# Kernel tuning notes

Measured on AMD Instinct MI355X. Metric: run time of the kernel, lower is better.

Reference implementation:

```python
import jax, jax.numpy as jnp
import numpy as np

B, N, D = 2, 256, 128

def _linear(x, W, b):
    # torch nn.Linear: y = x @ W.T + b, W shape (out, in)
    return jnp.einsum('bijd,od->bijo', x, W) + b

def setup_inputs() -> dict:
    key = jax.random.key(0)
    ks = jax.random.split(key, 11)
    s = 0.02
    inp = {
        'ef': jax.random.normal(ks[0], (B, N, N, D), dtype=jnp.float32),
        'Wq': jax.random.normal(ks[1], (D, D), dtype=jnp.float32) * s,
        'bq': jax.random.normal(ks[2], (D,), dtype=jnp.float32) * s,
        'Wk': jax.random.normal(ks[3], (D, D), dtype=jnp.float32) * s,
        'bk': jax.random.normal(ks[4], (D,), dtype=jnp.float32) * s,
        'Wv1': jax.random.normal(ks[5], (D, D), dtype=jnp.float32) * s,
        'bv1': jax.random.normal(ks[6], (D,), dtype=jnp.float32) * s,
        'Wv2': jax.random.normal(ks[7], (D, D), dtype=jnp.float32) * s,
        'bv2': jax.random.normal(ks[8], (D,), dtype=jnp.float32) * s,
        'Wo': jax.random.normal(ks[9], (D, D), dtype=jnp.float32) * s,
        'bo': jax.random.normal(ks[10], (D,), dtype=jnp.float32) * s,
    }
    return inp

def reference(ef, Wq, bq, Wk, bk, Wv1, bv1, Wv2, bv2, Wo, bo):
    d = ef.shape[-1]
    q = _linear(ef, Wq, bq)    # (b,i,l,d)
    k = _linear(ef, Wk, bk)    # (b,l,j,d)
    v1 = _linear(ef, Wv1, bv1) # (b,i,l,d)
    v2 = _linear(ef, Wv2, bv2) # (b,l,j,d)
    # scores over triples (i,l,j): sum_d q[b,i,l,d]*k[b,l,j,d]
    scale = jnp.asarray(1.0 / (d ** 0.5), dtype=ef.dtype)
    qk = jnp.einsum('bild,bljd->bilj', q, k) * scale
    # original softmax is over dim=-2 of (b,i,l,j,1) -> over j
    a = jax.nn.softmax(qk, axis=-1)  # (b,i,l,j)
    # sum_j a[b,i,l,j] * v1[b,i,l,d] * v2[b,l,j,d]
    ctx = jnp.einsum('bilj,bljd->bild', a, v2) * v1  # (b,i,l,d)
    out = _linear(ctx, Wo, bo)
    return out
```

## Files before the change

### kernel.cpp

```cpp
#include <hip/hip_runtime.h>


typedef __bf16 bf16x8 __attribute__((ext_vector_type(8)));
typedef float  f32x4  __attribute__((ext_vector_type(4)));

#define MFMA(a, b, c) __builtin_amdgcn_mfma_f32_16x16x32_bf16((a), (b), (c), 0, 0, 0)

union U8 { bf16x8 v; unsigned int w[4]; };

__device__ __forceinline__ unsigned short rne_bf16(float f) {
  unsigned int u = __float_as_uint(f);
  u += 0x7fffu + ((u >> 16) & 1u);
  return (unsigned short)(u >> 16);
}

__device__ __forceinline__ unsigned int cvt_pk(float lo, float hi) {
  unsigned int r;
  asm("v_cvt_pk_bf16_f32 %0, %1, %2" : "=v"(r) : "v"(lo), "v"(hi));
  return r;
}

__device__ __forceinline__ bf16x8 cvt_frag(const float* __restrict__ p) {
  f32x4 a = *(const f32x4*)p;
  f32x4 b = *(const f32x4*)(p + 4);
  U8 t;
  t.w[0] = cvt_pk(a[0], a[1]);
  t.w[1] = cvt_pk(a[2], a[3]);
  t.w[2] = cvt_pk(b[0], b[1]);
  t.w[3] = cvt_pk(b[2], b[3]);
  return t.v;
}

__device__ __forceinline__ bf16x8 xpose(unsigned int w01a, unsigned int w01b,
                                        unsigned int w23a, unsigned int w23b,
                                        int sa, int sb, bool hi) {
  U8 u;
  { int x0 = __shfl((int)w01a, sa), x1 = __shfl((int)w01b, sa);
    u.w[0] = (unsigned int)(hi ? x1 : x0); }
  { int x0 = __shfl((int)w23a, sa), x1 = __shfl((int)w23b, sa);
    u.w[1] = (unsigned int)(hi ? x1 : x0); }
  { int x0 = __shfl((int)w01a, sb), x1 = __shfl((int)w01b, sb);
    u.w[2] = (unsigned int)(hi ? x1 : x0); }
  { int x0 = __shfl((int)w23a, sb), x1 = __shfl((int)w23b, sb);
    u.w[3] = (unsigned int)(hi ? x1 : x0); }
  return u.v;
}

__device__ __forceinline__ void softmax_pack(f32x4 ST[16], unsigned int p01[16],
                                             unsigned int p23[16]) {
  float t16[16];
  #pragma unroll
  for (int jt = 0; jt < 16; ++jt)
    t16[jt] = fmaxf(fmaxf(ST[jt][0], ST[jt][1]), fmaxf(ST[jt][2], ST[jt][3]));
  #pragma unroll
  for (int s = 8; s >= 1; s >>= 1)
    #pragma unroll
    for (int k = 0; k < 16; ++k) if (k < s) t16[k] = fmaxf(t16[k], t16[k + s]);
  float mx = t16[0];
  mx = fmaxf(mx, __shfl_xor(mx, 16));
  mx = fmaxf(mx, __shfl_xor(mx, 32));

  float s16[16];
  #pragma unroll
  for (int jt = 0; jt < 16; ++jt) {
    float e0 = __expf(ST[jt][0] - mx);
    float e1 = __expf(ST[jt][1] - mx);
    float e2 = __expf(ST[jt][2] - mx);
    float e3 = __expf(ST[jt][3] - mx);
    ST[jt][0] = e0; ST[jt][1] = e1; ST[jt][2] = e2; ST[jt][3] = e3;
    s16[jt] = (e0 + e1) + (e2 + e3);
  }
  #pragma unroll
  for (int s = 8; s >= 1; s >>= 1)
    #pragma unroll
    for (int k = 0; k < 16; ++k) if (k < s) s16[k] += s16[k + s];
  float sm = s16[0];
  sm += __shfl_xor(sm, 16);
  sm += __shfl_xor(sm, 32);
  const float inv = 1.0f / sm;

  #pragma unroll
  for (int jt = 0; jt < 16; ++jt) {
    p01[jt] = cvt_pk(ST[jt][0] * inv, ST[jt][1] * inv);
    p23[jt] = cvt_pk(ST[jt][2] * inv, ST[jt][3] * inv);
  }
}

__global__ void cvt_weights(const float* __restrict__ Wq, const float* __restrict__ Wk,
                            const float* __restrict__ Wv1, const float* __restrict__ Wv2,
                            const float* __restrict__ Wo, unsigned short* __restrict__ ws) {
  int t = blockIdx.x * 256 + threadIdx.x;
  ws[t]             = rne_bf16(Wq[t]);
  ws[16384 + t]     = rne_bf16(Wk[t]);
  ws[2 * 16384 + t] = rne_bf16(Wv1[t]);
  ws[3 * 16384 + t] = rne_bf16(Wv2[t]);
  ws[4 * 16384 + t] = rne_bf16(Wo[t]);
}

__global__ __launch_bounds__(512, 2)
void edge_attn_kernel(const float* __restrict__ ef,
                      const unsigned short* __restrict__ wbf,
                      const float* __restrict__ bq, const float* __restrict__ bk,
                      const float* __restrict__ bv1, const float* __restrict__ bv2,
                      const float* __restrict__ bo,
                      float* __restrict__ out) {
  __shared__ unsigned short Kb[256 * 128];
  __shared__ unsigned short V2t[128 * 256];

  const int tid  = threadIdx.x;
  const int lane = tid & 63;
  const int wv   = tid >> 6;
  const int lc   = lane & 15;
  const int q4   = lane >> 4;
  const int bb   = blockIdx.x >> 8;
  const int lb   = blockIdx.x & 255;

  const unsigned short* WqB  = wbf;
  const unsigned short* WkB  = wbf + 16384;
  const unsigned short* Wv1B = wbf + 2 * 16384;
  const unsigned short* Wv2B = wbf + 3 * 16384;
  const unsigned short* WoB  = wbf + 4 * 16384;

  const f32x4 Z4 = {0.f, 0.f, 0.f, 0.f};
  const int jA = wv * 16;
  const int jB = wv * 16 + 128;

  {
    const float* Frow = ef + ((size_t)(bb * 256 + lb)) * (256 * 128);
    bf16x8 aFA[4], aFB[4];
    {
      const float* rpA = Frow + (jA + lc) * 128 + q4 * 8;
      const float* rpB = Frow + (jB + lc) * 128 + q4 * 8;
      #pragma unroll
      for (int kc = 0; kc < 4; ++kc) {
        aFA[kc] = cvt_frag(rpA + kc * 32);
        aFB[kc] = cvt_frag(rpB + kc * 32);
      }
    }

    f32x4 aKA[8], aVA[8], aKB[8], aVB[8];
    #pragma unroll
    for (int n = 0; n < 8; ++n) { aKA[n] = Z4; aVA[n] = Z4; aKB[n] = Z4; aVB[n] = Z4; }
    #pragma unroll
    for (int kc = 0; kc < 4; ++kc) {
      #pragma unroll
      for (int n = 0; n < 8; ++n) {
        bf16x8 bwk = *(const bf16x8*)(WkB  + (n * 16 + lc) * 128 + kc * 32 + q4 * 8);
        bf16x8 bwv = *(const bf16x8*)(Wv2B + (n * 16 + lc) * 128 + kc * 32 + q4 * 8);
        aKA[n] = MFMA(aFA[kc], bwk, aKA[n]);
        aKB[n] = MFMA(aFB[kc], bwk, aKB[n]);
        aVA[n] = MFMA(aFA[kc], bwv, aVA[n]);
        aVB[n] = MFMA(aFB[kc], bwv, aVB[n]);
      }
    }
    #pragma unroll
    for (int n = 0; n < 8; ++n) {
      const int o = n * 16 + lc;
      const float bkv = bk[o];
      const float bvv = bv2[o];
      #pragma unroll
      for (int r = 0; r < 4; ++r) {
        const int ja = jA + q4 * 4 + r;
        const int jb = jB + q4 * 4 + r;
        Kb[ja * 128 + (((o >> 3) ^ (ja & 15)) << 3) + (o & 7)] = rne_bf16(aKA[n][r] + bkv);
        Kb[jb * 128 + (((o >> 3) ^ (jb & 15)) << 3) + (o & 7)] = rne_bf16(aKB[n][r] + bkv);
        V2t[o * 256 + (((ja >> 3) ^ lc) << 3) + (ja & 7)]      = rne_bf16(aVA[n][r] + bvv);
        V2t[o * 256 + (((jb >> 3) ^ lc) << 3) + (jb & 7)]      = rne_bf16(aVB[n][r] + bvv);
      }
    }
  }
  __syncthreads();

  const float scale = 0.08838834764831845f;

  bf16x8 aEA[4], aEB[4];
  {
    const float* rpA = ef + (((size_t)(bb * 256 + jA + lc)) * 256 + lb) * 128 + q4 * 8;
    const float* rpB = ef + (((size_t)(bb * 256 + jB + lc)) * 256 + lb) * 128 + q4 * 8;
    f32x4 eA[8], eB[8];
    #pragma unroll
    for (int kc = 0; kc < 4; ++kc) {
      eA[2 * kc]     = *(const f32x4*)(rpA + kc * 32);
      eA[2 * kc + 1] = *(const f32x4*)(rpA + kc * 32 + 4);
      eB[2 * kc]     = *(const f32x4*)(rpB + kc * 32);
      eB[2 * kc + 1] = *(const f32x4*)(rpB + kc * 32 + 4);
    }
    #pragma unroll
    for (int kc = 0; kc < 4; ++kc) {
      U8 u;
      u.w[0] = cvt_pk(eA[2 * kc][0], eA[2 * kc][1]);
      u.w[1] = cvt_pk(eA[2 * kc][2], eA[2 * kc][3]);
      u.w[2] = cvt_pk(eA[2 * kc + 1][0], eA[2 * kc + 1][1]);
      u.w[3] = cvt_pk(eA[2 * kc + 1][2], eA[2 * kc + 1][3]);
      aEA[kc] = u.v;
      u.w[0] = cvt_pk(eB[2 * kc][0], eB[2 * kc][1]);
      u.w[1] = cvt_pk(eB[2 * kc][2], eB[2 * kc][3]);
      u.w[2] = cvt_pk(eB[2 * kc + 1][0], eB[2 * kc + 1][1]);
      u.w[3] = cvt_pk(eB[2 * kc + 1][2], eB[2 * kc + 1][3]);
      aEB[kc] = u.v;
    }
  }

  f32x4 QtA[8], QtB[8];
  #pragma unroll
  for (int nt = 0; nt < 8; ++nt) { QtA[nt] = Z4; QtB[nt] = Z4; }
  #pragma unroll
  for (int kc = 0; kc < 4; ++kc) {
    #pragma unroll
    for (int nt = 0; nt < 8; ++nt) {
      bf16x8 aW = *(const bf16x8*)(WqB + (nt * 16 + lc) * 128 + kc * 32 + q4 * 8);
      QtA[nt] = MFMA(aW, aEA[kc], QtA[nt]);
      QtB[nt] = MFMA(aW, aEB[kc], QtB[nt]);
    }
  }
  unsigned int qA01[8], qA23[8], qB01[8], qB23[8];
  #pragma unroll
  for (int nt = 0; nt < 8; ++nt) {
    f32x4 b4 = *(const f32x4*)(bq + nt * 16 + q4 * 4);
    qA01[nt] = cvt_pk((QtA[nt][0] + b4[0]) * scale, (QtA[nt][1] + b4[1]) * scale);
    qA23[nt] = cvt_pk((QtA[nt][2] + b4[2]) * scale, (QtA[nt][3] + b4[3]) * scale);
    qB01[nt] = cvt_pk((QtB[nt][0] + b4[0]) * scale, (QtB[nt][1] + b4[1]) * scale);
    qB23[nt] = cvt_pk((QtB[nt][2] + b4[2]) * scale, (QtB[nt][3] + b4[3]) * scale);
  }

  const int sa = ((2 * q4) & 3) * 16 + lc;
  const int sb = ((2 * q4 + 1) & 3) * 16 + lc;
  const bool hi = (q4 >= 2);

  bf16x8 bQA[4], bQB[4];
  #pragma unroll
  for (int kc = 0; kc < 4; ++kc) {
    bQA[kc] = xpose(qA01[2 * kc], qA01[2 * kc + 1], qA23[2 * kc], qA23[2 * kc + 1], sa, sb, hi);
    bQB[kc] = xpose(qB01[2 * kc], qB01[2 * kc + 1], qB23[2 * kc], qB23[2 * kc + 1], sa, sb, hi);
  }

  f32x4 SA[16], SB[16];
  #pragma unroll
  for (int jt = 0; jt < 16; ++jt) { SA[jt] = Z4; SB[jt] = Z4; }
  #pragma unroll
  for (int kc = 0; kc < 4; ++kc) {
    #pragma unroll
    for (int jt = 0; jt < 16; ++jt) {
      bf16x8 bK = *(const bf16x8*)(Kb + (jt * 16 + lc) * 128 + (((kc * 4 + q4) ^ lc) << 3));
      SA[jt] = MFMA(bK, bQA[kc], SA[jt]);
      SB[jt] = MFMA(bK, bQB[kc], SB[jt]);
    }
  }

  unsigned int pA01[16], pA23[16], pB01[16], pB23[16];
  softmax_pack(SA, pA01, pA23);
  softmax_pack(SB, pB01, pB23);

  bf16x8 aPA[8], aPB[8];
  #pragma unroll
  for (int kc = 0; kc < 8; ++kc) {
    aPA[kc] = xpose(pA01[2 * kc], pA01[2 * kc + 1], pA23[2 * kc], pA23[2 * kc + 1], sa, sb, hi);
    aPB[kc] = xpose(pB01[2 * kc], pB01[2 * kc + 1], pB23[2 * kc], pB23[2 * kc + 1], sa, sb, hi);
  }

  f32x4 CA[8], CB[8];
  #pragma unroll
  for (int nt = 0; nt < 8; ++nt) { CA[nt] = Z4; CB[nt] = Z4; }
  #pragma unroll
  for (int kc = 0; kc < 8; ++kc) {
    #pragma unroll
    for (int nt = 0; nt < 8; ++nt) {
      bf16x8 bV = *(const bf16x8*)(V2t + (nt * 16 + lc) * 256 + (((kc * 4 + q4) ^ lc) << 3));
      CA[nt] = MFMA(bV, aPA[kc], CA[nt]);
      CB[nt] = MFMA(bV, aPB[kc], CB[nt]);
    }
  }

  f32x4 VA[8], VB[8];
  #pragma unroll
  for (int nt = 0; nt < 8; ++nt) { VA[nt] = Z4; VB[nt] = Z4; }
  #pragma unroll
  for (int kc = 0; kc < 4; ++kc) {
    #pragma unroll
    for (int nt = 0; nt < 8; ++nt) {
      bf16x8 aW = *(const bf16x8*)(Wv1B + (nt * 16 + lc) * 128 + kc * 32 + q4 * 8);
      VA[nt] = MFMA(aW, aEA[kc], VA[nt]);
      VB[nt] = MFMA(aW, aEB[kc], VB[nt]);
    }
  }
  #pragma unroll
  for (int nt = 0; nt < 8; ++nt) {
    f32x4 b4 = *(const f32x4*)(bv1 + nt * 16 + q4 * 4);
    #pragma unroll
    for (int r = 0; r < 4; ++r) {
      CA[nt][r] *= (VA[nt][r] + b4[r]);
      CB[nt][r] *= (VB[nt][r] + b4[r]);
    }
  }

  unsigned int cA01[8], cA23[8], cB01[8], cB23[8];
  #pragma unroll
  for (int nt = 0; nt < 8; ++nt) {
    cA01[nt] = cvt_pk(CA[nt][0], CA[nt][1]);
    cA23[nt] = cvt_pk(CA[nt][2], CA[nt][3]);
    cB01[nt] = cvt_pk(CB[nt][0], CB[nt][1]);
    cB23[nt] = cvt_pk(CB[nt][2], CB[nt][3]);
  }
  bf16x8 aCA[4], aCB[4];
  #pragma unroll
  for (int kc = 0; kc < 4; ++kc) {
    aCA[kc] = xpose(cA01[2 * kc], cA01[2 * kc + 1], cA23[2 * kc], cA23[2 * kc + 1], sa, sb, hi);
    aCB[kc] = xpose(cB01[2 * kc], cB01[2 * kc + 1], cB23[2 * kc], cB23[2 * kc + 1], sa, sb, hi);
  }

  f32x4 OA[8], OB[8];
  #pragma unroll
  for (int n = 0; n < 8; ++n) { OA[n] = Z4; OB[n] = Z4; }
  #pragma unroll
  for (int kc = 0; kc < 4; ++kc) {
    #pragma unroll
    for (int n = 0; n < 8; ++n) {
      bf16x8 bw = *(const bf16x8*)(WoB + (n * 16 + lc) * 128 + kc * 32 + q4 * 8);
      OA[n] = MFMA(aCA[kc], bw, OA[n]);
      OB[n] = MFMA(aCB[kc], bw, OB[n]);
    }
  }
  #pragma unroll
  for (int n = 0; n < 8; ++n) {
    const float bov = bo[n * 16 + lc];
    #pragma unroll
    for (int r = 0; r < 4; ++r) {
      const int ia = jA + q4 * 4 + r;
      const int ib = jB + q4 * 4 + r;
      out[(((size_t)(bb * 256 + ia)) * 256 + lb) * 128 + n * 16 + lc] = OA[n][r] + bov;
      out[(((size_t)(bb * 256 + ib)) * 256 + lb) * 128 + n * 16 + lc] = OB[n][r] + bov;
    }
  }
}

extern "C" void kernel_launch(void* const* d_in, const int* in_sizes, int n_in,
                              void* d_out, int out_size, void* d_ws, size_t ws_size,
                              hipStream_t stream) {
  const float* ef   = (const float*)d_in[0];
  const float* Wq   = (const float*)d_in[1];
  const float* bqp  = (const float*)d_in[2];
  const float* Wk   = (const float*)d_in[3];
  const float* bkp  = (const float*)d_in[4];
  const float* Wv1  = (const float*)d_in[5];
  const float* bv1p = (const float*)d_in[6];
  const float* Wv2  = (const float*)d_in[7];
  const float* bv2p = (const float*)d_in[8];
  const float* Wo   = (const float*)d_in[9];
  const float* bop  = (const float*)d_in[10];
  unsigned short* wbf = (unsigned short*)d_ws;

  cvt_weights<<<64, 256, 0, stream>>>(Wq, Wk, Wv1, Wv2, Wo, wbf);
  edge_attn_kernel<<<512, 512, 0, stream>>>(ef, wbf, bqp, bkp, bv1p, bv2p, bop,
                                            (float*)d_out);
}
```

Baseline: 235.4 us.

## Spill V2 tile to global workspace to halve LDS and raise occupancy

```diff
diff --git a/kernel.cpp b/kernel.cpp
--- a/kernel.cpp
+++ b/kernel.cpp
@@ -3,10 +3,14 @@
 
 typedef __bf16 bf16x8 __attribute__((ext_vector_type(8)));
 typedef float  f32x4  __attribute__((ext_vector_type(4)));
+typedef unsigned short u16x4 __attribute__((ext_vector_type(4)));
 
 #define MFMA(a, b, c) __builtin_amdgcn_mfma_f32_16x16x32_bf16((a), (b), (c), 0, 0, 0)
 
 union U8 { bf16x8 v; unsigned int w[4]; };
+
+#define WS_V2T 81920
+static const size_t WS_NEEDED = (81920ull + 512ull * 32768ull) * 2ull;
 
 __device__ __forceinline__ unsigned short rne_bf16(float f) {
   unsigned int u = __float_as_uint(f);
@@ -97,15 +101,14 @@
   ws[4 * 16384 + t] = rne_bf16(Wo[t]);
 }
 
-__global__ __launch_bounds__(512, 2)
+__global__ __launch_bounds__(512, 4)
 void edge_attn_kernel(const float* __restrict__ ef,
-                      const unsigned short* __restrict__ wbf,
+                      unsigned short* __restrict__ ws,
                       const float* __restrict__ bq, const float* __restrict__ bk,
                       const float* __restrict__ bv1, const float* __restrict__ bv2,
                       const float* __restrict__ bo,
                       float* __restrict__ out) {
   __shared__ unsigned short Kb[256 * 128];
-  __shared__ unsigned short V2t[128 * 256];
 
   const int tid  = threadIdx.x;
   const int lane = tid & 63;
@@ -115,6 +118,261 @@
   const int bb   = blockIdx.x >> 8;
   const int lb   = blockIdx.x & 255;
 
+  const unsigned short* WqB  = ws;
+  const unsigned short* WkB  = ws + 16384;
+  const unsigned short* Wv1B = ws + 2 * 16384;
+  const unsigned short* Wv2B = ws + 3 * 16384;
+  const unsigned short* WoB  = ws + 4 * 16384;
+  unsigned short* vsl = ws + WS_V2T + ((size_t)(bb * 256 + lb)) * 32768;
+
+  const f32x4 Z4 = {0.f, 0.f, 0.f, 0.f};
+  const int jA = wv * 16;
+  const int jB = wv * 16 + 128;
+
+  {
+    const float* Frow = ef + ((size_t)(bb * 256 + lb)) * (256 * 128);
+    bf16x8 aFA[4], aFB[4];
+    {
+      const float* rpA = Frow + (jA + lc) * 128 + q4 * 8;
+      const float* rpB = Frow + (jB + lc) * 128 + q4 * 8;
+      #pragma unroll
+      for (int kc = 0; kc < 4; ++kc) {
+        aFA[kc] = cvt_frag(rpA + kc * 32);
+        aFB[kc] = cvt_frag(rpB + kc * 32);
+      }
+    }
+
+    {
+      f32x4 kA[8], kB[8];
+      #pragma unroll
+      for (int n = 0; n < 8; ++n) { kA[n] = Z4; kB[n] = Z4; }
+      #pragma unroll
+      for (int kc = 0; kc < 4; ++kc) {
+        #pragma unroll
+        for (int n = 0; n < 8; ++n) {
+          bf16x8 bwk = *(const bf16x8*)(WkB + (n * 16 + lc) * 128 + kc * 32 + q4 * 8);
+          kA[n] = MFMA(aFA[kc], bwk, kA[n]);
+          kB[n] = MFMA(aFB[kc], bwk, kB[n]);
+        }
+      }
+      #pragma unroll
+      for (int n = 0; n < 8; ++n) {
+        const int o = n * 16 + lc;
+        const float bkv = bk[o];
+        #pragma unroll
+        for (int r = 0; r < 4; ++r) {
+          const int ja = jA + q4 * 4 + r;
+          const int jb = jB + q4 * 4 + r;
+          Kb[ja * 128 + (((o >> 3) ^ (ja & 15)) << 3) + (o & 7)] = rne_bf16(kA[n][r] + bkv);
+          Kb[jb * 128 + (((o >> 3) ^ (jb & 15)) << 3) + (o & 7)] = rne_bf16(kB[n][r] + bkv);
+        }
+      }
+    }
+
+    {
+      f32x4 vA[8], vB[8];
+      #pragma unroll
+      for (int n = 0; n < 8; ++n) { vA[n] = Z4; vB[n] = Z4; }
+      #pragma unroll
+      for (int kc = 0; kc < 4; ++kc) {
+        #pragma unroll
+        for (int n = 0; n < 8; ++n) {
+          bf16x8 bwv = *(const bf16x8*)(Wv2B + (n * 16 + lc) * 128 + kc * 32 + q4 * 8);
+          vA[n] = MFMA(aFA[kc], bwv, vA[n]);
+          vB[n] = MFMA(aFB[kc], bwv, vB[n]);
+        }
+      }
+      #pragma unroll
+      for (int n = 0; n < 8; ++n) {
+        const int o = n * 16 + lc;
+        const float bvv = bv2[o];
+        u16x4 pkA, pkB;
+        #pragma unroll
+        for (int r = 0; r < 4; ++r) {
+          pkA[r] = rne_bf16(vA[n][r] + bvv);
+          pkB[r] = rne_bf16(vB[n][r] + bvv);
+        }
+        *(u16x4*)(vsl + o * 256 + jA + q4 * 4) = pkA;
+        *(u16x4*)(vsl + o * 256 + jB + q4 * 4) = pkB;
+      }
+    }
+  }
+
+  f32x4 e0[8];
+  {
+    const float* rp = ef + (((size_t)(bb * 256 + wv * 16 + lc)) * 256 + lb) * 128 + q4 * 8;
+    #pragma unroll
+    for (int kc = 0; kc < 4; ++kc) {
+      e0[2 * kc]     = *(const f32x4*)(rp + kc * 32);
+      e0[2 * kc + 1] = *(const f32x4*)(rp + kc * 32 + 4);
+    }
+  }
+  __syncthreads();
+
+  const float scale = 0.08838834764831845f;
+  const int sa = ((2 * q4) & 3) * 16 + lc;
+  const int sb = ((2 * q4 + 1) & 3) * 16 + lc;
+  const bool hi = (q4 >= 2);
+
+  #pragma unroll
+  for (int h = 0; h < 2; ++h) {
+    const int i0 = wv * 16 + h * 128;
+
+    bf16x8 aE[4];
+    {
+      f32x4 eH[8];
+      if (h == 0) {
+        #pragma unroll
+        for (int k = 0; k < 8; ++k) eH[k] = e0[k];
+      } else {
+        const float* rp = ef + (((size_t)(bb * 256 + i0 + lc)) * 256 + lb) * 128 + q4 * 8;
+        #pragma unroll
+        for (int kc = 0; kc < 4; ++kc) {
+          eH[2 * kc]     = *(const f32x4*)(rp + kc * 32);
+          eH[2 * kc + 1] = *(const f32x4*)(rp + kc * 32 + 4);
+        }
+      }
+      #pragma unroll
+      for (int kc = 0; kc < 4; ++kc) {
+        U8 u;
+        u.w[0] = cvt_pk(eH[2 * kc][0], eH[2 * kc][1]);
+        u.w[1] = cvt_pk(eH[2 * kc][2], eH[2 * kc][3]);
+        u.w[2] = cvt_pk(eH[2 * kc + 1][0], eH[2 * kc + 1][1]);
+        u.w[3] = cvt_pk(eH[2 * kc + 1][2], eH[2 * kc + 1][3]);
+        aE[kc] = u.v;
+      }
+    }
+
+    bf16x8 bQ[4];
+    {
+      f32x4 Qt[8];
+      #pragma unroll
+      for (int nt = 0; nt < 8; ++nt) Qt[nt] = Z4;
+      #pragma unroll
+      for (int kc = 0; kc < 4; ++kc) {
+        #pragma unroll
+        for (int nt = 0; nt < 8; ++nt) {
+          bf16x8 aW = *(const bf16x8*)(WqB + (nt * 16 + lc) * 128 + kc * 32 + q4 * 8);
+          Qt[nt] = MFMA(aW, aE[kc], Qt[nt]);
+        }
+      }
+      unsigned int q01[8], q23[8];
+      #pragma unroll
+      for (int nt = 0; nt < 8; ++nt) {
+        f32x4 b4 = *(const f32x4*)(bq + nt * 16 + q4 * 4);
+        q01[nt] = cvt_pk((Qt[nt][0] + b4[0]) * scale, (Qt[nt][1] + b4[1]) * scale);
+        q23[nt] = cvt_pk((Qt[nt][2] + b4[2]) * scale, (Qt[nt][3] + b4[3]) * scale);
+      }
+      #pragma unroll
+      for (int kc = 0; kc < 4; ++kc)
+        bQ[kc] = xpose(q01[2 * kc], q01[2 * kc + 1], q23[2 * kc], q23[2 * kc + 1], sa, sb, hi);
+    }
+
+    bf16x8 aP[8];
+    {
+      f32x4 S[16];
+      #pragma unroll
+      for (int jt = 0; jt < 16; ++jt) S[jt] = Z4;
+      #pragma unroll
+      for (int kc = 0; kc < 4; ++kc) {
+        #pragma unroll
+        for (int jt = 0; jt < 16; ++jt) {
+          bf16x8 bK = *(const bf16x8*)(Kb + (jt * 16 + lc) * 128 + (((kc * 4 + q4) ^ lc) << 3));
+          S[jt] = MFMA(bK, bQ[kc], S[jt]);
+        }
+      }
+      unsigned int p01[16], p23[16];
+      softmax_pack(S, p01, p23);
+      #pragma unroll
+      for (int kc = 0; kc < 8; ++kc)
+        aP[kc] = xpose(p01[2 * kc], p01[2 * kc + 1], p23[2 * kc], p23[2 * kc + 1], sa, sb, hi);
+    }
+
+    f32x4 Ct[8];
+    #pragma unroll
+    for (int nt = 0; nt < 8; ++nt) Ct[nt] = Z4;
+    #pragma unroll
+    for (int kc = 0; kc < 8; ++kc) {
+      #pragma unroll
+      for (int nt = 0; nt < 8; ++nt) {
+        bf16x8 bV = *(const bf16x8*)(vsl + (nt * 16 + lc) * 256 + kc * 32 + q4 * 8);
+        Ct[nt] = MFMA(bV, aP[kc], Ct[nt]);
+      }
+    }
+
+    {
+      f32x4 Vt[8];
+      #pragma unroll
+      for (int nt = 0; nt < 8; ++nt) Vt[nt] = Z4;
+      #pragma unroll
+      for (int kc = 0; kc < 4; ++kc) {
+        #pragma unroll
+        for (int nt = 0; nt < 8; ++nt) {
+          bf16x8 aW = *(const bf16x8*)(Wv1B + (nt * 16 + lc) * 128 + kc * 32 + q4 * 8);
+          Vt[nt] = MFMA(aW, aE[kc], Vt[nt]);
+        }
+      }
+      #pragma unroll
+      for (int nt = 0; nt < 8; ++nt) {
+        f32x4 b4 = *(const f32x4*)(bv1 + nt * 16 + q4 * 4);
+        #pragma unroll
+        for (int r = 0; r < 4; ++r) Ct[nt][r] *= (Vt[nt][r] + b4[r]);
+      }
+    }
+
+    bf16x8 aC[4];
+    {
+      unsigned int c01[8], c23[8];
+      #pragma unroll
+      for (int nt = 0; nt < 8; ++nt) {
+        c01[nt] = cvt_pk(Ct[nt][0], Ct[nt][1]);
+        c23[nt] = cvt_pk(Ct[nt][2], Ct[nt][3]);
+      }
+      #pragma unroll
+      for (int kc = 0; kc < 4; ++kc)
+        aC[kc] = xpose(c01[2 * kc], c01[2 * kc + 1], c23[2 * kc], c23[2 * kc + 1], sa, sb, hi);
+    }
+    f32x4 O[8];
+    #pragma unroll
+    for (int n = 0; n < 8; ++n) O[n] = Z4;
+    #pragma unroll
+    for (int kc = 0; kc < 4; ++kc) {
+      #pragma unroll
+      for (int n = 0; n < 8; ++n) {
+        bf16x8 bw = *(const bf16x8*)(WoB + (n * 16 + lc) * 128 + kc * 32 + q4 * 8);
+        O[n] = MFMA(aC[kc], bw, O[n]);
+      }
+    }
+    #pragma unroll
+    for (int n = 0; n < 8; ++n) {
+      const float bov = bo[n * 16 + lc];
+      #pragma unroll
+      for (int r = 0; r < 4; ++r) {
+        const int i = i0 + q4 * 4 + r;
+        out[(((size_t)(bb * 256 + i)) * 256 + lb) * 128 + n * 16 + lc] = O[n][r] + bov;
+      }
+    }
+  }
+}
+
+__global__ __launch_bounds__(512, 2)
+void edge_attn_r4(const float* __restrict__ ef,
+                  const unsigned short* __restrict__ wbf,
+                  const float* __restrict__ bq, const float* __restrict__ bk,
+                  const float* __restrict__ bv1, const float* __restrict__ bv2,
+                  const float* __restrict__ bo,
+                  float* __restrict__ out) {
+  __shared__ unsigned short Kb[256 * 128];
+  __shared__ unsigned short V2t[128 * 256];
+
+  const int tid  = threadIdx.x;
+  const int lane = tid & 63;
+  const int wv   = tid >> 6;
+  const int lc   = lane & 15;
+  const int q4   = lane >> 4;
+  const int bb   = blockIdx.x >> 8;
+  const int lb   = blockIdx.x & 255;
+
   const unsigned short* WqB  = wbf;
   const unsigned short* WkB  = wbf + 16384;
   const unsigned short* Wv1B = wbf + 2 * 16384;
@@ -137,7 +395,6 @@
         aFB[kc] = cvt_frag(rpB + kc * 32);
       }
     }
-
     f32x4 aKA[8], aVA[8], aKB[8], aVB[8];
     #pragma unroll
     for (int n = 0; n < 8; ++n) { aKA[n] = Z4; aVA[n] = Z4; aKB[n] = Z4; aVB[n] = Z4; }
@@ -172,7 +429,6 @@
   __syncthreads();
 
   const float scale = 0.08838834764831845f;
-
   bf16x8 aEA[4], aEB[4];
   {
     const float* rpA = ef + (((size_t)(bb * 256 + jA + lc)) * 256 + lb) * 128 + q4 * 8;
@@ -350,6 +606,12 @@
   unsigned short* wbf = (unsigned short*)d_ws;
 
   cvt_weights<<<64, 256, 0, stream>>>(Wq, Wk, Wv1, Wv2, Wo, wbf);
-  edge_attn_kernel<<<512, 512, 0, stream>>>(ef, wbf, bqp, bkp, bv1p, bv2p, bop,
-                                            (float*)d_out);
-}
+
+  if (ws_size >= WS_NEEDED) {
+    edge_attn_kernel<<<512, 512, 0, stream>>>(ef, wbf, bqp, bkp, bv1p, bv2p, bop,
+                                              (float*)d_out);
+  } else {
+    edge_attn_r4<<<512, 512, 0, stream>>>(ef, wbf, bqp, bkp, bv1p, bv2p, bop,
+                                          (float*)d_out);
+  }
+}
```

Result: slower. 489.9 us (+108.1%).
